# Performance work log

Measured on AMD Instinct MI355X. Metric: run time of the kernel, lower is better.

## Reference

```python
import jax, jax.numpy as jnp
import numpy as np

N_INV, N_FUND = 100000, 20000
D_INV, D_FUND, H = 128, 64, 128
E, EL = 600000, 200000


def setup_inputs() -> dict:
    key = jax.random.key(0)
    ks = jax.random.split(key, 26)
    f = lambda k, shape: (jax.random.normal(k, shape, dtype=jnp.float32) * 0.05)
    inp = {
        'x_inv': jax.random.normal(ks[0], (N_INV, D_INV), dtype=jnp.float32),
        'x_fund': jax.random.normal(ks[1], (N_FUND, D_FUND), dtype=jnp.float32),
        'src_if': jax.random.randint(ks[2], (E,), 0, N_INV),
        'dst_if': jax.random.randint(ks[3], (E,), 0, N_FUND),
        'src_fi': jax.random.randint(ks[4], (E,), 0, N_FUND),
        'dst_fi': jax.random.randint(ks[5], (E,), 0, N_INV),
        'eli_inv': jax.random.randint(ks[6], (EL,), 0, N_INV),
        'eli_fund': jax.random.randint(ks[7], (EL,), 0, N_FUND),
        # layer-1 SAGEConv weights per relation (PyG: out = lin_l(mean(x_j)) + lin_r(x_dst))
        'W1l_if': f(ks[8], (H, D_INV)), 'b1_if': jnp.zeros((H,), jnp.float32), 'W1r_if': f(ks[9], (H, D_FUND)),
        'W1l_fi': f(ks[10], (H, D_FUND)), 'b1_fi': jnp.zeros((H,), jnp.float32), 'W1r_fi': f(ks[11], (H, D_INV)),
        # layer-2 SAGEConv weights per relation
        'W2l_if': f(ks[12], (H, H)), 'b2_if': jnp.zeros((H,), jnp.float32), 'W2r_if': f(ks[13], (H, H)),
        'W2l_fi': f(ks[14], (H, H)), 'b2_fi': jnp.zeros((H,), jnp.float32), 'W2r_fi': f(ks[15], (H, H)),
        # link predictor MLP
        'Wp1': f(ks[16], (H, 2 * H)), 'bp1': jnp.zeros((H,), jnp.float32),
        'Wp2': f(ks[17], (1, H)), 'bp2': jnp.zeros((1,), jnp.float32),
    }
    return inp


def _sage(x_src, x_dst, src, dst, n_dst, Wl, bl, Wr):
    # mean-aggregate neighbor messages, then lin_l(mean) + bias + lin_r(root)
    msg = x_src[src]                                              # [E, d_src]
    s = jax.ops.segment_sum(msg, dst, num_segments=n_dst)         # [n_dst, d_src]
    cnt = jax.ops.segment_sum(jnp.ones((src.shape[0],), x_src.dtype), dst, num_segments=n_dst)
    mean = s / jnp.maximum(cnt, 1.0)[:, None]                     # isolated nodes -> 0
    return mean @ Wl.T + bl + x_dst @ Wr.T


def reference(x_inv, x_fund, src_if, dst_if, src_fi, dst_fi, eli_inv, eli_fund,
              W1l_if, b1_if, W1r_if, W1l_fi, b1_fi, W1r_fi,
              W2l_if, b2_if, W2r_if, W2l_fi, b2_fi, W2r_fi,
              Wp1, bp1, Wp2, bp2):
    # layer 1 (hetero: one incoming relation per node type, aggr='sum' is identity)
    h_fund = jax.nn.relu(_sage(x_inv, x_fund, src_if, dst_if, N_FUND, W1l_if, b1_if, W1r_if))
    h_inv = jax.nn.relu(_sage(x_fund, x_inv, src_fi, dst_fi, N_INV, W1l_fi, b1_fi, W1r_fi))
    # layer 2
    z_fund = _sage(h_inv, h_fund, src_if, dst_if, N_FUND, W2l_if, b2_if, W2r_if)
    z_inv = _sage(h_fund, h_inv, src_fi, dst_fi, N_INV, W2l_fi, b2_fi, W2r_fi)
    # link predictor
    xi = z_inv[eli_inv]                                           # [EL, H]
    xj = z_fund[eli_fund]                                         # [EL, H]
    x = jnp.concatenate([xi, xj], axis=-1)                        # [EL, 2H]
    x = jax.nn.relu(x @ Wp1.T + bp1)
    return jax.nn.sigmoid(x @ Wp2.T + bp2)                        # [EL, 1]
```

## Files before the change

### kernel.cpp

```cpp
#include <hip/hip_runtime.h>
#include <cstdint>
#include <cstddef>

namespace {

typedef short bf16x8 __attribute__((ext_vector_type(8)));
typedef float f32x4 __attribute__((ext_vector_type(4)));

constexpr int kNInv  = 100000;
constexpr int kNFund = 20000;
constexpr int kH     = 128;
constexpr int kE     = 600000;
constexpr int kEL    = 200000;

constexpr int kW1lIF = 0;
constexpr int kW1rIF = 16384;
constexpr int kW1lFI = 24576;
constexpr int kW1rFI = 32768;
constexpr int kWTot  = 49152;

constexpr int kCW2lFI = 0;
constexpr int kCW2rFI = 16384;
constexpr int kCW2lIF = 32768;
constexpr int kCW2rIF = 49152;

__device__ __forceinline__ float bf_lo(uint32_t u) {
  union { uint32_t i; float f; } v; v.i = u << 16; return v.f;
}
__device__ __forceinline__ float bf_hi(uint32_t u) {
  union { uint32_t i; float f; } v; v.i = u & 0xffff0000u; return v.f;
}
__device__ __forceinline__ ushort f2bf(float f) {
  union { float f; uint32_t i; } v; v.f = f;
  uint32_t x = v.i;
  return (ushort)((x + 0x7fffu + ((x >> 16) & 1u)) >> 16);
}

constexpr int kXiQ = kNInv * 128 / 4;
constexpr int kXfQ = kNFund * 64 / 4;
constexpr int kWQ  = kWTot / 4;
constexpr int kTotQ = kXiQ + kXfQ + kWQ;
constexpr int kZF = kNFund / 4;
constexpr int kZI = kNInv / 4;
constexpr int kTotQ2 = kTotQ + kZF + kZI;
constexpr int kConvB2 = (kTotQ2 + 255) / 256;

__device__ void convert_body(int q, const float* __restrict__ xi, const float* __restrict__ xf,
                             const float* w0, const float* w1, const float* w2, const float* w3,
                             ushort* __restrict__ xi_b, ushort* __restrict__ xf_b,
                             ushort* __restrict__ wa,
                             int* __restrict__ deg_fund, int* __restrict__ deg_inv) {
  if (q >= kTotQ2) return;
  if (q >= kTotQ) {
    const int z = q - kTotQ;
    if (z < kZF) ((int4*)deg_fund)[z] = make_int4(0, 0, 0, 0);
    else ((int4*)deg_inv)[z - kZF] = make_int4(0, 0, 0, 0);
    return;
  }
  const float* src;
  ushort* dst;
  int sidx, didx;
  if (q < kXiQ) {
    src = xi; dst = xi_b; sidx = q * 4; didx = q * 4;
  } else if (q < kXiQ + kXfQ) {
    src = xf; dst = xf_b; sidx = (q - kXiQ) * 4; didx = sidx;
  } else {
    const int e = (q - kXiQ - kXfQ) * 4;
    const float* ws[4] = {w0, w1, w2, w3};
    const int beg[5] = {kW1lIF, kW1rIF, kW1lFI, kW1rFI, kWTot};
    int s = 0;
    while (e >= beg[s + 1]) ++s;
    src = ws[s]; dst = wa; sidx = e - beg[s]; didx = e;
  }
  float4 v = *(const float4*)(src + sidx);
  ushort4 o = make_ushort4(f2bf(v.x), f2bf(v.y), f2bf(v.z), f2bf(v.w));
  *(ushort4*)(dst + didx) = o;
}

__device__ void composite_body(int b, const float* __restrict__ Wp1,
                               const float* __restrict__ W2l_fi, const float* __restrict__ W2r_fi,
                               const float* __restrict__ W2l_if, const float* __restrict__ W2r_if,
                               const float* __restrict__ b2_fi, const float* __restrict__ b2_if,
                               const float* __restrict__ bp1,
                               ushort* __restrict__ cw, float* __restrict__ bu_inv,
                               float* __restrict__ bu_fund, float* sA ) {
  const int tid = threadIdx.x;
  if (b == 16) {
    if (tid < 128) {
      float s = 0.f;
      for (int j = 0; j < 128; ++j) s += Wp1[(size_t)tid * 256 + j] * b2_fi[j];
      bu_inv[tid] = s;
    } else {
      const int o = tid - 128;
      float s = bp1[o];
      for (int j = 0; j < 128; ++j) s += Wp1[(size_t)o * 256 + 128 + j] * b2_if[j];
      bu_fund[o] = s;
    }
    return;
  }
  const int m = b >> 2;
  const int rb = (b & 3) * 32;
  const float* A = Wp1 + (m >= 2 ? 128 : 0);
  const float* B = (m == 0) ? W2l_fi : (m == 1) ? W2r_fi : (m == 2) ? W2l_if : W2r_if;
  for (int i = tid; i < 32 * 128; i += 256) {
    const int r = i >> 7, c = i & 127;
    sA[r * 132 + c] = A[(size_t)(rb + r) * 256 + c];
  }
  __syncthreads();
  const int lr = tid >> 3;
  const int k0 = (tid & 7) * 16;
  float acc[16];
#pragma unroll
  for (int i = 0; i < 16; ++i) acc[i] = 0.f;
  for (int j = 0; j < 128; ++j) {
    const float a = sA[lr * 132 + j];
    const float* Brow = B + (size_t)j * 128 + k0;
#pragma unroll
    for (int i = 0; i < 16; i += 4) {
      float4 v = *(const float4*)(Brow + i);
      acc[i] += a * v.x; acc[i + 1] += a * v.y; acc[i + 2] += a * v.z; acc[i + 3] += a * v.w;
    }
  }
  ushort* dst = cw + (size_t)m * 16384 + (size_t)(rb + lr) * 128 + k0;
  ushort ov[16];
#pragma unroll
  for (int i = 0; i < 16; ++i) ov[i] = f2bf(acc[i]);
#pragma unroll
  for (int i = 0; i < 16; i += 4)
    *(ushort4*)(dst + i) = *(const ushort4*)(ov + i);
}

__global__ __launch_bounds__(256) void prep(
    const float* xi, const float* xf,
    const float* w0, const float* w1, const float* w2, const float* w3,
    ushort* xi_b, ushort* xf_b, ushort* wa,
    int* deg_fund, int* deg_inv,
    const float* Wp1, const float* W2l_fi, const float* W2r_fi,
    const float* W2l_if, const float* W2r_if,
    const float* b2_fi, const float* b2_if, const float* bp1,
    ushort* cw, float* bu_inv, float* bu_fund) {
  __shared__ float smem[32 * 132];
  const int b = blockIdx.x;
  if (b < kConvB2) {
    convert_body(b * 256 + threadIdx.x, xi, xf, w0, w1, w2, w3, xi_b, xf_b, wa,
                 deg_fund, deg_inv);
  } else {
    composite_body(b - kConvB2, Wp1, W2l_fi, W2r_fi, W2l_if, W2r_if,
                   b2_fi, b2_if, bp1, cw, bu_inv, bu_fund, smem);
  }
}

__global__ void count_rank2(const int* __restrict__ d0, int* __restrict__ g0,
                            int* __restrict__ r0v,
                            const int* __restrict__ d1, int* __restrict__ g1,
                            int* __restrict__ r1v, int n) {
  int e = blockIdx.x * blockDim.x + threadIdx.x;
  if (e < n) {
    r0v[e] = atomicAdd(&g0[d0[e]], 1);
  } else if (e < 2 * n) {
    int ee = e - n;
    r1v[ee] = atomicAdd(&g1[d1[ee]], 1);
  }
}


__device__ __forceinline__ void scan_partial_body(const int* __restrict__ deg,
                                                  int* __restrict__ bsum, int n, int blk) {
  __shared__ int red[256];
  const int tid = threadIdx.x;
  const int base = blk * 1024 + tid * 4;
  int s = 0;
  if (base + 3 < n) {
    int4 v = *(const int4*)(deg + base);
    s = v.x + v.y + v.z + v.w;
  } else {
    for (int i = 0; i < 4; ++i)
      if (base + i < n) s += deg[base + i];
  }
  red[tid] = s;
  __syncthreads();
  for (int d = 128; d > 0; d >>= 1) {
    if (tid < d) red[tid] += red[tid + d];
    __syncthreads();
  }
  if (tid == 0) bsum[blk] = red[0];
}

__global__ void scan_partial2(const int* __restrict__ degF, int* __restrict__ bsumF, int nF, int nbF,
                              const int* __restrict__ degI, int* __restrict__ bsumI, int nI) {
  if ((int)blockIdx.x < nbF) scan_partial_body(degF, bsumF, nF, blockIdx.x);
  else scan_partial_body(degI, bsumI, nI, blockIdx.x - nbF);
}

__device__ __forceinline__ void scan_small_body(int* __restrict__ bsum, int nb) {
  __shared__ int sh[1024];
  const int tid = threadIdx.x;
  const int v = (tid < nb) ? bsum[tid] : 0;
  sh[tid] = v;
  __syncthreads();
  for (int d = 1; d < 1024; d <<= 1) {
    int t = (tid >= d) ? sh[tid - d] : 0;
    __syncthreads();
    sh[tid] += t;
    __syncthreads();
  }
  if (tid < nb) bsum[tid] = sh[tid] - v;
}

__global__ void scan_small2(int* __restrict__ bsumF, int nbF, int* __restrict__ bsumI, int nbI) {
  if (blockIdx.x == 0) scan_small_body(bsumF, nbF);
  else scan_small_body(bsumI, nbI);
}

__device__ __forceinline__ void scan_apply_body(const int* __restrict__ deg,
                                                const int* __restrict__ bsum,
                                                int* __restrict__ off, int n, int blk) {
  __shared__ int red[256];
  const int tid = threadIdx.x;
  const int base = blk * 1024 + tid * 4;
  int v[4] = {0, 0, 0, 0};
  const bool full = (base + 3 < n);
  if (full) {
    int4 t = *(const int4*)(deg + base);
    v[0] = t.x; v[1] = t.y; v[2] = t.z; v[3] = t.w;
  } else {
    for (int i = 0; i < 4; ++i)
      if (base + i < n) v[i] = deg[base + i];
  }
  const int s = v[0] + v[1] + v[2] + v[3];
  red[tid] = s;
  __syncthreads();
  for (int d = 1; d < 256; d <<= 1) {
    int t = (tid >= d) ? red[tid - d] : 0;
    __syncthreads();
    red[tid] += t;
    __syncthreads();
  }
  int o[4];
  o[0] = bsum[blk] + red[tid] - s;
  o[1] = o[0] + v[0];
  o[2] = o[1] + v[1];
  o[3] = o[2] + v[2];
  if (full) {
    *(int4*)(off + base) = make_int4(o[0], o[1], o[2], o[3]);
  } else {
    for (int i = 0; i < 4; ++i)
      if (base + i < n) off[base + i] = o[i];
  }
#pragma unroll
  for (int i = 0; i < 4; ++i)
    if (base + i == n - 1) off[n] = o[i] + v[i];
}

__global__ void scan_apply2(const int* __restrict__ degF, const int* __restrict__ bsumF,
                            int* __restrict__ offF, int nF, int nbF,
                            const int* __restrict__ degI, const int* __restrict__ bsumI,
                            int* __restrict__ offI, int nI) {
  if ((int)blockIdx.x < nbF) scan_apply_body(degF, bsumF, offF, nF, blockIdx.x);
  else scan_apply_body(degI, bsumI, offI, nI, blockIdx.x - nbF);
}

__global__ void fill2(const int* __restrict__ s0, const int* __restrict__ d0,
                      const int* __restrict__ r0v, const int* __restrict__ off0,
                      int* __restrict__ c0,
                      const int* __restrict__ s1, const int* __restrict__ d1,
                      const int* __restrict__ r1v, const int* __restrict__ off1,
                      int* __restrict__ c1, int n) {
  int e = blockIdx.x * blockDim.x + threadIdx.x;
  if (e < n) {
    c0[off0[d0[e]] + r0v[e]] = s0[e];
  } else if (e < 2 * n) {
    int ee = e - n;
    c1[off1[d1[ee]] + r1v[ee]] = s1[ee];
  }
}


__device__ __forceinline__ void acc8w(float* a, uint4 u, float w) {
  a[0] = fmaf(w, bf_lo(u.x), a[0]); a[1] = fmaf(w, bf_hi(u.x), a[1]);
  a[2] = fmaf(w, bf_lo(u.y), a[2]); a[3] = fmaf(w, bf_hi(u.y), a[3]);
  a[4] = fmaf(w, bf_lo(u.z), a[4]); a[5] = fmaf(w, bf_hi(u.z), a[5]);
  a[6] = fmaf(w, bf_lo(u.w), a[6]); a[7] = fmaf(w, bf_hi(u.w), a[7]);
}

template <int D, int DEP>
__device__ __forceinline__ void mean_node(const ushort* __restrict__ xsrc,
                                          const int* __restrict__ csr,
                                          const int* __restrict__ off,
                                          ushort* __restrict__ mean, int node, int lane) {
  constexpr int NSUB = (D == 128) ? 4 : 8;
  const int sub = (D == 128) ? (lane >> 4) : (lane >> 3);
  const int ll  = (D == 128) ? (lane & 15) : (lane & 7);
  const size_t co = (size_t)ll * 8;
  const int lo = off[node], hi = off[node + 1];
  float a[8] = {0.f, 0.f, 0.f, 0.f, 0.f, 0.f, 0.f, 0.f};
  for (int e0 = lo + sub; e0 < hi; e0 += NSUB * DEP) {
    int idx[DEP];
    float w[DEP];
#pragma unroll
    for (int j = 0; j < DEP; ++j) {
      const int e = e0 + NSUB * j;
      idx[j] = csr[min(e, hi - 1)];
      w[j] = (e < hi) ? 1.0f : 0.0f;
    }
    uint4 u[DEP];
#pragma unroll
    for (int j = 0; j < DEP; ++j)
      u[j] = *(const uint4*)(xsrc + (size_t)idx[j] * D + co);
#pragma unroll
    for (int j = 0; j < DEP; ++j) acc8w(a, u[j], w[j]);
  }
#pragma unroll
  for (int i = 0; i < 8; ++i) {
    if (D == 64) a[i] += __shfl_xor(a[i], 8);
    a[i] += __shfl_xor(a[i], 16);
    a[i] += __shfl_xor(a[i], 32);
  }
  if (sub == 0) {
    const float sc = (hi > lo) ? 1.0f / (float)(hi - lo) : 0.0f;
    ushort o8[8];
#pragma unroll
    for (int i = 0; i < 8; ++i) o8[i] = f2bf(a[i] * sc);
    *(uint4*)(mean + (size_t)node * D + co) = *(const uint4*)o8;
  }
}

template <int DA, int DEPA, int DB, int DEPB>
__global__ void sage_mean_dual(const ushort* __restrict__ xA, const int* __restrict__ csrA,
                               const int* __restrict__ offA, ushort* __restrict__ outA, int nA,
                               const ushort* __restrict__ xB, const int* __restrict__ csrB,
                               const int* __restrict__ offB, ushort* __restrict__ outB, int nB) {
  const int wave = (int)((blockIdx.x * blockDim.x + threadIdx.x) >> 6);
  const int lane = threadIdx.x & 63;
  if (wave < nA) mean_node<DA, DEPA>(xA, csrA, offA, outA, wave, lane);
  else if (wave < nA + nB) mean_node<DB, DEPB>(xB, csrB, offB, outB, wave - nA, lane);
}


template <int D1, int D2>
__device__ void gemm_body(const ushort* __restrict__ A1, const ushort* __restrict__ A2,
                          const ushort* __restrict__ W1, const ushort* __restrict__ W2,
                          const float* __restrict__ bias, int act,
                          ushort* __restrict__ out, int n, int blk, ushort* lds) {
  constexpr int K1 = D1 / 32;
  constexpr int K2 = D2 / 32;
  constexpr int CH1 = 128 * D1 / 8;
  constexpr int CHT = 128 * (D1 + D2) / 8;

  const int tid = threadIdx.x;
  const int wid = tid >> 6;
  const int lane = tid & 63;
  const int lo16 = lane & 15;
  const int hi4 = lane >> 4;
  const int row0 = blk * 128 + wid * 32;

  const int r0 = min(row0 + lo16, n - 1);
  const int r1 = min(row0 + 16 + lo16, n - 1);

  bf16x8 aA[2][K1], aB[2][K2];
  {
    const ushort* a0p = A1 + (size_t)r0 * D1 + hi4 * 8;
    const ushort* a1p = A1 + (size_t)r1 * D1 + hi4 * 8;
#pragma unroll
    for (int k = 0; k < K1; ++k) {
      aA[0][k] = *(const bf16x8*)(a0p + k * 32);
      aA[1][k] = *(const bf16x8*)(a1p + k * 32);
    }
    const ushort* b0p = A2 + (size_t)r0 * D2 + hi4 * 8;
    const ushort* b1p = A2 + (size_t)r1 * D2 + hi4 * 8;
#pragma unroll
    for (int k = 0; k < K2; ++k) {
      aB[0][k] = *(const bf16x8*)(b0p + k * 32);
      aB[1][k] = *(const bf16x8*)(b1p + k * 32);
    }
  }

#pragma unroll
  for (int it = 0; it < CHT / 256; ++it) {
    const int c = it * 256 + tid;
    const int g = c * 8;
    bf16x8 v;
    int dest;
    if (g < 128 * D1) {
      const int row = g / D1, col = g % D1;
      v = *(const bf16x8*)(W1 + g);
      dest = ((col >> 5) * 8 + (row >> 4)) * 64 + (((col >> 3) & 3) << 4) + (row & 15);
    } else {
      const int g2 = g - 128 * D1;
      const int row = g2 / D2, col = g2 % D2;
      v = *(const bf16x8*)(W2 + g2);
      dest = CH1 + ((col >> 5) * 8 + (row >> 4)) * 64 + (((col >> 3) & 3) << 4) + (row & 15);
    }
    *((bf16x8*)lds + dest) = v;
  }
  __syncthreads();

  f32x4 acc[2][8];
#pragma unroll
  for (int rt = 0; rt < 2; ++rt)
#pragma unroll
    for (int ct = 0; ct < 8; ++ct)
      acc[rt][ct] = (f32x4){0.f, 0.f, 0.f, 0.f};

  const bf16x8* fr = (const bf16x8*)lds;
#pragma unroll
  for (int k = 0; k < K1; ++k) {
#pragma unroll
    for (int ct = 0; ct < 8; ++ct) {
      bf16x8 w = fr[(k * 8 + ct) * 64 + lane];
      acc[0][ct] = __builtin_amdgcn_mfma_f32_16x16x32_bf16(w, aA[0][k], acc[0][ct], 0, 0, 0);
      acc[1][ct] = __builtin_amdgcn_mfma_f32_16x16x32_bf16(w, aA[1][k], acc[1][ct], 0, 0, 0);
    }
  }
#pragma unroll
  for (int k = 0; k < K2; ++k) {
#pragma unroll
    for (int ct = 0; ct < 8; ++ct) {
      bf16x8 w = fr[CH1 + (k * 8 + ct) * 64 + lane];
      acc[0][ct] = __builtin_amdgcn_mfma_f32_16x16x32_bf16(w, aB[0][k], acc[0][ct], 0, 0, 0);
      acc[1][ct] = __builtin_amdgcn_mfma_f32_16x16x32_bf16(w, aB[1][k], acc[1][ct], 0, 0, 0);
    }
  }

  const int colb = hi4 * 4;
#pragma unroll
  for (int rt = 0; rt < 2; ++rt) {
    const int row = row0 + rt * 16 + lo16;
    if (row < n) {
#pragma unroll
      for (int ct = 0; ct < 8; ++ct) {
        float b4[4];
        *(float4*)b4 = *(const float4*)(bias + ct * 16 + colb);
        ushort o[4];
#pragma unroll
        for (int j = 0; j < 4; ++j) {
          float x = acc[rt][ct][j] + b4[j];
          if (act) x = fmaxf(x, 0.f);
          o[j] = f2bf(x);
        }
        *(ushort4*)(out + (size_t)row * kH + ct * 16 + colb) = *(const ushort4*)o;
      }
    }
  }
}

__global__ __launch_bounds__(256) void gemm_stage1(
    const ushort* A1f, const ushort* A2f, const ushort* W1f, const ushort* W2f,
    const float* biasf, ushort* outf, int nf, int nbf,
    const ushort* A1i, const ushort* A2i, const ushort* W1i, const ushort* W2i,
    const float* biasi, ushort* outi, int ni) {
  __shared__ ushort lds[128 * 192];
  if ((int)blockIdx.x < nbf)
    gemm_body<128, 64>(A1f, A2f, W1f, W2f, biasf, 1, outf, nf, blockIdx.x, lds);
  else
    gemm_body<64, 128>(A1i, A2i, W1i, W2i, biasi, 1, outi, ni, blockIdx.x - nbf, lds);
}

__global__ __launch_bounds__(256) void gemm_stage2(
    const ushort* A1f, const ushort* A2f, const ushort* W1f, const ushort* W2f,
    const float* biasf, ushort* outf, int nf, int nbf,
    const ushort* A1i, const ushort* A2i, const ushort* W1i, const ushort* W2i,
    const float* biasi, ushort* outi, int ni) {
  __shared__ ushort lds[128 * 256];
  if ((int)blockIdx.x < nbf)
    gemm_body<128, 128>(A1f, A2f, W1f, W2f, biasf, 0, outf, nf, blockIdx.x, lds);
  else
    gemm_body<128, 128>(A1i, A2i, W1i, W2i, biasi, 0, outi, ni, blockIdx.x - nbf, lds);
}


__global__ void link_pred(const ushort* __restrict__ u_inv, const ushort* __restrict__ u_fund,
                          const int* __restrict__ ei, const int* __restrict__ ej,
                          const float* __restrict__ Wp2, const float* __restrict__ bp2,
                          float* __restrict__ out, int nl) {
  const int wave = (int)((blockIdx.x * blockDim.x + threadIdx.x) >> 6);
  const int lane = threadIdx.x & 63;
  const int q = lane >> 4, l16 = lane & 15;
  const int link = wave * 4 + q;
  if (link >= nl) return;
  const int i = ei[link];
  const int j = ej[link];
  uint4 ua = *(const uint4*)(u_inv + (size_t)i * 128 + l16 * 8);
  uint4 ub = *(const uint4*)(u_fund + (size_t)j * 128 + l16 * 8);
  float4 w0 = *(const float4*)(Wp2 + l16 * 8);
  float4 w1 = *(const float4*)(Wp2 + l16 * 8 + 4);
  float p = fmaxf(bf_lo(ua.x) + bf_lo(ub.x), 0.f) * w0.x
          + fmaxf(bf_hi(ua.x) + bf_hi(ub.x), 0.f) * w0.y
          + fmaxf(bf_lo(ua.y) + bf_lo(ub.y), 0.f) * w0.z
          + fmaxf(bf_hi(ua.y) + bf_hi(ub.y), 0.f) * w0.w
          + fmaxf(bf_lo(ua.z) + bf_lo(ub.z), 0.f) * w1.x
          + fmaxf(bf_hi(ua.z) + bf_hi(ub.z), 0.f) * w1.y
          + fmaxf(bf_lo(ua.w) + bf_lo(ub.w), 0.f) * w1.z
          + fmaxf(bf_hi(ua.w) + bf_hi(ub.w), 0.f) * w1.w;
#pragma unroll
  for (int o = 8; o > 0; o >>= 1) p += __shfl_xor(p, o);
  if (l16 == 0) out[link] = 1.0f / (1.0f + expf(-(p + bp2[0])));
}

}

extern "C" void kernel_launch(void* const* d_in, const int* in_sizes, int n_in,
                              void* d_out, int out_size, void* d_ws, size_t ws_size,
                              hipStream_t stream) {
  const float* x_inv  = (const float*)d_in[0];
  const float* x_fund = (const float*)d_in[1];
  const int* src_if   = (const int*)d_in[2];
  const int* dst_if   = (const int*)d_in[3];
  const int* src_fi   = (const int*)d_in[4];
  const int* dst_fi   = (const int*)d_in[5];
  const int* eli_inv  = (const int*)d_in[6];
  const int* eli_fund = (const int*)d_in[7];
  const float* W1l_if = (const float*)d_in[8];
  const float* b1_if  = (const float*)d_in[9];
  const float* W1r_if = (const float*)d_in[10];
  const float* W1l_fi = (const float*)d_in[11];
  const float* b1_fi  = (const float*)d_in[12];
  const float* W1r_fi = (const float*)d_in[13];
  const float* W2l_if = (const float*)d_in[14];
  const float* b2_if  = (const float*)d_in[15];
  const float* W2r_if = (const float*)d_in[16];
  const float* W2l_fi = (const float*)d_in[17];
  const float* b2_fi  = (const float*)d_in[18];
  const float* W2r_fi = (const float*)d_in[19];
  const float* Wp1    = (const float*)d_in[20];
  const float* bp1    = (const float*)d_in[21];
  const float* Wp2    = (const float*)d_in[22];
  const float* bp2    = (const float*)d_in[23];
  float* out = (float*)d_out;

  char* p = (char*)d_ws;
  auto alloc = [&](size_t bytes) -> void* {
    void* r = (void*)p;
    p += (bytes + 255) & ~(size_t)255;
    return r;
  };
  int* deg_fund = (int*)alloc((size_t)kNFund * 4);
  int* deg_inv  = (int*)alloc((size_t)kNInv * 4);
  int* off_fund = (int*)alloc((size_t)(kNFund + 1) * 4);
  int* off_inv  = (int*)alloc((size_t)(kNInv + 1) * 4);
  int* bsumF    = (int*)alloc((size_t)1024 * 4);
  int* bsumI    = (int*)alloc((size_t)1024 * 4);
  int* rank_if  = (int*)alloc((size_t)kE * 4);
  int* rank_fi  = (int*)alloc((size_t)kE * 4);
  int* csr_if   = (int*)alloc((size_t)kE * 4);
  int* csr_fi   = (int*)alloc((size_t)kE * 4);
  ushort* xi_b = (ushort*)alloc((size_t)kNInv * 128 * 2);
  ushort* xf_b = (ushort*)alloc((size_t)kNFund * 64 * 2);
  ushort* wa   = (ushort*)alloc((size_t)kWTot * 2);
  ushort* cw   = (ushort*)alloc((size_t)4 * 16384 * 2);
  float* bu_inv  = (float*)alloc((size_t)128 * 4);
  float* bu_fund = (float*)alloc((size_t)128 * 4);
  ushort* bufA = (ushort*)alloc((size_t)kNFund * 128 * 2);
  ushort* bufB = (ushort*)alloc((size_t)kNFund * 128 * 2);
  ushort* bufC = (ushort*)alloc((size_t)kNInv * 128 * 2);
  ushort* bufD = (ushort*)alloc((size_t)kNInv * 128 * 2);
  ushort* bufE = (ushort*)alloc((size_t)kNFund * 128 * 2);
  ushort* bufF = (ushort*)alloc((size_t)kNInv * 128 * 2);

  const int TB = 256;
  const int nbFund = (kNFund + 1023) / 1024;
  const int nbInv  = (kNInv + 1023) / 1024;
  const int gemmF = (kNFund + 127) / 128;
  const int gemmI = (kNInv + 127) / 128;

  prep<<<kConvB2 + 17, 256, 0, stream>>>(
      x_inv, x_fund, W1l_if, W1r_if, W1l_fi, W1r_fi, xi_b, xf_b, wa,
      deg_fund, deg_inv,
      Wp1, W2l_fi, W2r_fi, W2l_if, W2r_if, b2_fi, b2_if, bp1, cw, bu_inv, bu_fund);

  count_rank2<<<(2 * kE + TB - 1) / TB, TB, 0, stream>>>(
      dst_if, deg_fund, rank_if, dst_fi, deg_inv, rank_fi, kE);

  scan_partial2<<<nbFund + nbInv, 256, 0, stream>>>(deg_fund, bsumF, kNFund, nbFund,
                                                    deg_inv, bsumI, kNInv);
  scan_small2<<<2, 1024, 0, stream>>>(bsumF, nbFund, bsumI, nbInv);
  scan_apply2<<<nbFund + nbInv, 256, 0, stream>>>(deg_fund, bsumF, off_fund, kNFund, nbFund,
                                                  deg_inv, bsumI, off_inv, kNInv);

  fill2<<<(2 * kE + TB - 1) / TB, TB, 0, stream>>>(
      src_if, dst_if, rank_if, off_fund, csr_if,
      src_fi, dst_fi, rank_fi, off_inv, csr_fi, kE);

  const int meanBlocks = (kNFund + kNInv + 3) / 4;

  sage_mean_dual<128, 4, 64, 2><<<meanBlocks, 256, 0, stream>>>(
      xi_b, csr_if, off_fund, bufA, kNFund, xf_b, csr_fi, off_inv, bufC, kNInv);
  gemm_stage1<<<gemmF + gemmI, 256, 0, stream>>>(
      bufA, xf_b, wa + kW1lIF, wa + kW1rIF, b1_if, bufB, kNFund, gemmF,
      bufC, xi_b, wa + kW1lFI, wa + kW1rFI, b1_fi, bufD, kNInv);
  sage_mean_dual<128, 4, 128, 2><<<meanBlocks, 256, 0, stream>>>(
      bufD, csr_if, off_fund, bufA, kNFund, bufB, csr_fi, off_inv, bufC, kNInv);
  gemm_stage2<<<gemmF + gemmI, 256, 0, stream>>>(
      bufA, bufB, cw + kCW2lIF, cw + kCW2rIF, bu_fund, bufE, kNFund, gemmF,
      bufC, bufD, cw + kCW2lFI, cw + kCW2rFI, bu_inv, bufF, kNInv);
  link_pred<<<(kEL / 4 + 3) / 4, 256, 0, stream>>>(bufF, bufE, eli_inv, eli_fund,
                                                   Wp2, bp2, out, kEL);
}
```

Baseline: 303.0 us.

## Fold degree counting into prep kernel and drop the small scan kernel

Moves the per-edge atomic degree counting and rank assignment into the prep kernel as extra blocks, with degree zeroing done by memset beforehand instead of in the convert blocks. Removes the separate block-sum scan kernel by having each scan_apply block reduce the preceding block sums itself. Two kernel launches and their serialization gaps are removed. The cost is redundant block-sum reads in scan_apply and two extra memset operations.

```diff
diff --git a/kernel.cpp b/kernel.cpp
--- a/kernel.cpp
+++ b/kernel.cpp
@@ -40,23 +40,26 @@
 constexpr int kXfQ = kNFund * 64 / 4;
 constexpr int kWQ  = kWTot / 4;
 constexpr int kTotQ = kXiQ + kXfQ + kWQ;
-constexpr int kZF = kNFund / 4;
-constexpr int kZI = kNInv / 4;
-constexpr int kTotQ2 = kTotQ + kZF + kZI;
-constexpr int kConvB2 = (kTotQ2 + 255) / 256;
+constexpr int kConvB = kTotQ / 256;
+constexpr int kCountB = (2 * kE + 255) / 256;
+
+__device__ __forceinline__ void count_body(int e,
+                                           const int* __restrict__ dst_if,
+                                           int* __restrict__ deg_fund, int* __restrict__ rank_if,
+                                           const int* __restrict__ dst_fi,
+                                           int* __restrict__ deg_inv, int* __restrict__ rank_fi) {
+  if (e < kE) {
+    rank_if[e] = atomicAdd(&deg_fund[dst_if[e]], 1);
+  } else if (e < 2 * kE) {
+    const int ee = e - kE;
+    rank_fi[ee] = atomicAdd(&deg_inv[dst_fi[ee]], 1);
+  }
+}
 
 __device__ void convert_body(int q, const float* __restrict__ xi, const float* __restrict__ xf,
                              const float* w0, const float* w1, const float* w2, const float* w3,
                              ushort* __restrict__ xi_b, ushort* __restrict__ xf_b,
-                             ushort* __restrict__ wa,
-                             int* __restrict__ deg_fund, int* __restrict__ deg_inv) {
-  if (q >= kTotQ2) return;
-  if (q >= kTotQ) {
-    const int z = q - kTotQ;
-    if (z < kZF) ((int4*)deg_fund)[z] = make_int4(0, 0, 0, 0);
-    else ((int4*)deg_inv)[z - kZF] = make_int4(0, 0, 0, 0);
-    return;
-  }
+                             ushort* __restrict__ wa) {
   const float* src;
   ushort* dst;
   int sidx, didx;
@@ -131,35 +134,24 @@
 }
 
 __global__ __launch_bounds__(256) void prep(
+    const int* dst_if, int* deg_fund, int* rank_if,
+    const int* dst_fi, int* deg_inv, int* rank_fi,
     const float* xi, const float* xf,
     const float* w0, const float* w1, const float* w2, const float* w3,
     ushort* xi_b, ushort* xf_b, ushort* wa,
-    int* deg_fund, int* deg_inv,
     const float* Wp1, const float* W2l_fi, const float* W2r_fi,
     const float* W2l_if, const float* W2r_if,
     const float* b2_fi, const float* b2_if, const float* bp1,
     ushort* cw, float* bu_inv, float* bu_fund) {
   __shared__ float smem[32 * 132];
   const int b = blockIdx.x;
-  if (b < kConvB2) {
-    convert_body(b * 256 + threadIdx.x, xi, xf, w0, w1, w2, w3, xi_b, xf_b, wa,
-                 deg_fund, deg_inv);
+  if (b < kCountB) {
+    count_body(b * 256 + threadIdx.x, dst_if, deg_fund, rank_if, dst_fi, deg_inv, rank_fi);
+  } else if (b < kCountB + kConvB) {
+    convert_body((b - kCountB) * 256 + threadIdx.x, xi, xf, w0, w1, w2, w3, xi_b, xf_b, wa);
   } else {
-    composite_body(b - kConvB2, Wp1, W2l_fi, W2r_fi, W2l_if, W2r_if,
+    composite_body(b - kCountB - kConvB, Wp1, W2l_fi, W2r_fi, W2l_if, W2r_if,
                    b2_fi, b2_if, bp1, cw, bu_inv, bu_fund, smem);
-  }
-}
-
-__global__ void count_rank2(const int* __restrict__ d0, int* __restrict__ g0,
-                            int* __restrict__ r0v,
-                            const int* __restrict__ d1, int* __restrict__ g1,
-                            int* __restrict__ r1v, int n) {
-  int e = blockIdx.x * blockDim.x + threadIdx.x;
-  if (e < n) {
-    r0v[e] = atomicAdd(&g0[d0[e]], 1);
-  } else if (e < 2 * n) {
-    int ee = e - n;
-    r1v[ee] = atomicAdd(&g1[d1[ee]], 1);
   }
 }
 
@@ -192,31 +184,25 @@
   else scan_partial_body(degI, bsumI, nI, blockIdx.x - nbF);
 }
 
-__device__ __forceinline__ void scan_small_body(int* __restrict__ bsum, int nb) {
-  __shared__ int sh[1024];
-  const int tid = threadIdx.x;
-  const int v = (tid < nb) ? bsum[tid] : 0;
-  sh[tid] = v;
-  __syncthreads();
-  for (int d = 1; d < 1024; d <<= 1) {
-    int t = (tid >= d) ? sh[tid - d] : 0;
-    __syncthreads();
-    sh[tid] += t;
-    __syncthreads();
-  }
-  if (tid < nb) bsum[tid] = sh[tid] - v;
-}
-
-__global__ void scan_small2(int* __restrict__ bsumF, int nbF, int* __restrict__ bsumI, int nbI) {
-  if (blockIdx.x == 0) scan_small_body(bsumF, nbF);
-  else scan_small_body(bsumI, nbI);
-}
-
 __device__ __forceinline__ void scan_apply_body(const int* __restrict__ deg,
                                                 const int* __restrict__ bsum,
                                                 int* __restrict__ off, int n, int blk) {
   __shared__ int red[256];
+  __shared__ int sbase;
   const int tid = threadIdx.x;
+  int part = 0;
+  for (int i = tid; i < blk; i += 256) part += bsum[i];
+  red[tid] = part;
+  __syncthreads();
+  for (int d = 128; d > 0; d >>= 1) {
+    if (tid < d) red[tid] += red[tid + d];
+    __syncthreads();
+  }
+  if (tid == 0) sbase = red[0];
+  __syncthreads();
+  const int base0 = sbase;
+  __syncthreads();
+
   const int base = blk * 1024 + tid * 4;
   int v[4] = {0, 0, 0, 0};
   const bool full = (base + 3 < n);
@@ -237,7 +223,7 @@
     __syncthreads();
   }
   int o[4];
-  o[0] = bsum[blk] + red[tid] - s;
+  o[0] = base0 + red[tid] - s;
   o[1] = o[0] + v[0];
   o[2] = o[1] + v[1];
   o[3] = o[2] + v[2];
@@ -563,17 +549,16 @@
   const int gemmF = (kNFund + 127) / 128;
   const int gemmI = (kNInv + 127) / 128;
 
-  prep<<<kConvB2 + 17, 256, 0, stream>>>(
+  hipMemsetAsync(deg_fund, 0, (size_t)kNFund * 4, stream);
+  hipMemsetAsync(deg_inv, 0, (size_t)kNInv * 4, stream);
+
+  prep<<<kCountB + kConvB + 17, 256, 0, stream>>>(
+      dst_if, deg_fund, rank_if, dst_fi, deg_inv, rank_fi,
       x_inv, x_fund, W1l_if, W1r_if, W1l_fi, W1r_fi, xi_b, xf_b, wa,
-      deg_fund, deg_inv,
       Wp1, W2l_fi, W2r_fi, W2l_if, W2r_if, b2_fi, b2_if, bp1, cw, bu_inv, bu_fund);
-
-  count_rank2<<<(2 * kE + TB - 1) / TB, TB, 0, stream>>>(
-      dst_if, deg_fund, rank_if, dst_fi, deg_inv, rank_fi, kE);
 
   scan_partial2<<<nbFund + nbInv, 256, 0, stream>>>(deg_fund, bsumF, kNFund, nbFund,
                                                     deg_inv, bsumI, kNInv);
-  scan_small2<<<2, 1024, 0, stream>>>(bsumF, nbFund, bsumI, nbInv);
   scan_apply2<<<nbFund + nbInv, 256, 0, stream>>>(deg_fund, bsumF, off_fund, kNFund, nbFund,
                                                   deg_inv, bsumI, off_inv, kNInv);
 
```

Measured after the change: 303.2 us. About the same (+0.1%).
